# Performance work log

Hardware: AMD Instinct MI355X
Metric: run time of the kernel (lower is better)

Reference implementation:

```python
import jax, jax.numpy as jnp
import numpy as np

B, L, H, D = 1, 2048, 24, 128
HID = H * D            # 3072
MLP = 4 * HID          # 12288
EPS = 1e-6


def setup_inputs() -> dict:
    key = jax.random.key(0)
    ks = jax.random.split(key, 8)
    w = lambda k, shape: jax.random.normal(k, shape, jnp.float32) * 0.02
    return {
        "x": jax.random.normal(ks[0], (B, L, HID), jnp.float32),
        "vec": jax.random.normal(ks[1], (B, HID), jnp.float32),
        "pe": jax.random.normal(ks[2], (1, 1, L, D // 2, 2, 2), jnp.float32),
        # Modulation(double=False): Dense(3*hidden)
        "mod_w": w(ks[3], (HID, 3 * HID)),
        "mod_b": jnp.zeros((3 * HID,), jnp.float32),
        # pre_norm LayerNormalization (gamma/beta)
        "ln_gamma": jnp.ones((HID,), jnp.float32),
        "ln_beta": jnp.zeros((HID,), jnp.float32),
        # linear1: Dense(3*hidden + mlp_hidden)
        "w1": w(ks[4], (HID, 3 * HID + MLP)),
        "b1": jnp.zeros((3 * HID + MLP,), jnp.float32),
        # QKNorm scales (per head_dim)
        "q_scale": jnp.ones((D,), jnp.float32),
        "k_scale": jnp.ones((D,), jnp.float32),
        # linear2: Dense(hidden), input hidden + mlp_hidden
        "w2": w(ks[5], (HID + MLP, HID)),
        "b2": jnp.zeros((HID,), jnp.float32),
    }


def _rmsnorm(t, scale):
    # RMSNorm over last (head) dim, eps=1e-6
    return t * jax.lax.rsqrt(jnp.mean(jnp.square(t), axis=-1, keepdims=True) + EPS) * scale


def _apply_rope(t, pe):
    # t: (B,H,L,D) -> view (B,H,L,D/2,1,2); pe: (1,1,L,D/2,2,2)
    t_ = t.reshape(*t.shape[:-1], -1, 1, 2)
    out = pe[..., 0] * t_[..., 0] + pe[..., 1] * t_[..., 1]  # (B,H,L,D/2,2)
    return out.reshape(t.shape)


def reference(x, vec, pe, mod_w, mod_b, ln_gamma, ln_beta, w1, b1,
              q_scale, k_scale, w2, b2):
    # Modulation: silu -> Dense -> split into shift/scale/gate, each [B,1,HID]
    mod = (jax.nn.silu(vec) @ mod_w + mod_b)[:, None, :]
    shift, scale, gate = jnp.split(mod, 3, axis=-1)

    # pre_norm LayerNorm (eps=1e-6) + modulation affine
    mu = jnp.mean(x, axis=-1, keepdims=True)
    var = jnp.mean(jnp.square(x - mu), axis=-1, keepdims=True)
    ln = (x - mu) * jax.lax.rsqrt(var + EPS) * ln_gamma + ln_beta
    x_mod = (1.0 + scale) * ln + shift

    # linear1 -> split qkv / mlp branches
    h = x_mod @ w1 + b1
    qkv, mlp = h[..., : 3 * HID], h[..., 3 * HID:]

    # 'B L (K H D) -> K B H L D'
    qkv = qkv.reshape(B, L, 3, H, D).transpose(2, 0, 3, 1, 4)
    q, k, v = qkv[0], qkv[1], qkv[2]

    # QK RMSNorm + RoPE
    q = _apply_rope(_rmsnorm(q, q_scale), pe)
    k = _apply_rope(_rmsnorm(k, k_scale), pe)

    # scaled dot-product attention
    scores = jnp.einsum("bhqd,bhkd->bhqk", q, k) * (D ** -0.5)
    attn = jnp.einsum("bhqk,bhkd->bhqd", jax.nn.softmax(scores, axis=-1), v)
    attn = attn.transpose(0, 2, 1, 3).reshape(B, L, HID)  # B H L D -> B L (H D)

    # concat attention + gelu(mlp, tanh approx) -> linear2, gated residual
    out = jnp.concatenate([attn, jax.nn.gelu(mlp, approximate=True)], axis=-1) @ w2 + b2
    return x + gate * out
```

## Files before the change

kernel.cpp:

```cpp
#include <hip/hip_runtime.h>
#include <hip/hip_bf16.h>
#include <cstdint>

#define L_SEQ 2048
#define NH    24
#define DH    128
#define HID   3072
#define MLPD  12288
#define N1    21504
#define K2    15360
#define EPSF  1e-6f
#define ATT_SCALE 0.08838834764831845f

typedef __bf16 bf16x8 __attribute__((ext_vector_type(8)));
typedef float  f32x4  __attribute__((ext_vector_type(4)));

__device__ __forceinline__ float gelu_tanh(float x) {
    float x3 = x * x * x;
    return 0.5f * x * (1.f + tanhf(0.7978845608028654f * (x + 0.044715f * x3)));
}

__device__ __forceinline__ unsigned short f2bf(float f) {
    union { float f; unsigned int u; } x{f};
    unsigned int r = x.u + 0x7fffu + ((x.u >> 16) & 1u);
    return (unsigned short)(r >> 16);
}

__device__ __forceinline__ void gload_lds16(const void* g, void* l) {
    __builtin_amdgcn_global_load_lds(
        (__attribute__((address_space(1))) void*)g,
        (__attribute__((address_space(3))) void*)l, 16, 0, 0);
}

__global__ __launch_bounds__(256)
void k_convT(const float* __restrict__ in, unsigned short* __restrict__ out,
             int R, int C) {
    __shared__ unsigned short s[64][72];
    const int r0 = blockIdx.y * 64, c0 = blockIdx.x * 64;
    const int tid = threadIdx.x;
    const int row = tid >> 4, c4 = (tid & 15) * 4;
    #pragma unroll
    for (int rr = 0; rr < 4; rr++) {
        int r = row + rr * 16;
        float4 v = *(const float4*)&in[(size_t)(r0 + r) * C + c0 + c4];
        s[r][c4 + 0] = f2bf(v.x); s[r][c4 + 1] = f2bf(v.y);
        s[r][c4 + 2] = f2bf(v.z); s[r][c4 + 3] = f2bf(v.w);
    }
    __syncthreads();
    #pragma unroll
    for (int rr = 0; rr < 4; rr++) {
        int oc = row + rr * 16;
        ushort4 t = make_ushort4(s[c4 + 0][oc], s[c4 + 1][oc],
                                 s[c4 + 2][oc], s[c4 + 3][oc]);
        *(ushort4*)&out[(size_t)(c0 + oc) * R + r0 + c4] = t;
    }
}

__global__ __launch_bounds__(256)
void k_mod(const float* __restrict__ vec, const float* __restrict__ mod_w,
           const float* __restrict__ mod_b, float* __restrict__ mod) {
    __shared__ float sv[384];
    const int j  = blockIdx.x * 256 + threadIdx.x;
    const int k0 = blockIdx.y * 384;
    for (int i = threadIdx.x; i < 384; i += 256) {
        float v = vec[k0 + i];
        sv[i] = v / (1.f + __expf(-v));
    }
    __syncthreads();
    float acc = (blockIdx.y == 0) ? mod_b[j] : 0.f;
    #pragma unroll 8
    for (int i = 0; i < 384; i++)
        acc = fmaf(sv[i], mod_w[(size_t)(k0 + i) * 9216 + j], acc);
    atomicAdd(&mod[j], acc);
}

__global__ __launch_bounds__(256)
void k_ln(const float* __restrict__ x, const float* __restrict__ mod,
          const float* __restrict__ gamma, const float* __restrict__ beta,
          unsigned short* __restrict__ x_mod) {
    __shared__ float rs_[4], rs2_[4];
    const int l = blockIdx.x, tid = threadIdx.x;
    const float* xr = x + (size_t)l * HID;
    float s = 0.f, s2 = 0.f;
    for (int i = tid; i < HID; i += 256) {
        float v = xr[i]; s += v; s2 = fmaf(v, v, s2);
    }
    #pragma unroll
    for (int off = 32; off; off >>= 1) { s += __shfl_xor(s, off); s2 += __shfl_xor(s2, off); }
    const int w = tid >> 6;
    if ((tid & 63) == 0) { rs_[w] = s; rs2_[w] = s2; }
    __syncthreads();
    s  = rs_[0] + rs_[1] + rs_[2] + rs_[3];
    s2 = rs2_[0] + rs2_[1] + rs2_[2] + rs2_[3];
    float mu   = s * (1.f / HID);
    float var  = s2 * (1.f / HID) - mu * mu;
    float rstd = rsqrtf(var + EPSF);
    unsigned short* orow = x_mod + (size_t)l * HID;
    for (int i = tid; i < HID; i += 256) {
        float ln = (xr[i] - mu) * rstd * gamma[i] + beta[i];
        orow[i] = f2bf(fmaf(1.f + mod[HID + i], ln, mod[i]));
    }
}

template<int MODE>
__global__ __launch_bounds__(512, 2)
void gemm8(const unsigned short* __restrict__ A,
           const unsigned short* __restrict__ Bt,
           const float* __restrict__ bias, int K, int nkt,
           float* __restrict__ qkv, unsigned short* __restrict__ vt,
           unsigned short* __restrict__ a2, float* __restrict__ part) {
    extern __shared__ unsigned short sm[];
    unsigned short* As = sm;
    unsigned short* Bs = sm + 32768;
    const int tid = threadIdx.x;
    const int w = tid >> 6, lane = tid & 63;
    const int wm = w >> 2, wn = w & 3;
    const int quad = lane >> 4, lr = lane & 15;
    const int bm = blockIdx.y * 256, bn = blockIdx.x * 256;
    const int koff = (MODE == 1) ? blockIdx.z * (K >> 1) : 0;

    f32x4 acc[8][4] = {};
    bf16x8 a_[4][2], b_[2][2];

#define STG(SEL, HM, KT, D) do {                                             \
    const unsigned short* gp_ = (SEL) ? Bt : A;                              \
    const int gb_ = (SEL) ? bn : bm;                                         \
    unsigned short* ls_ = ((SEL) ? Bs : As) + (D) * 16384 + (HM) * 8192      \
                          + ((tid & ~63) << 3);                              \
    _Pragma("unroll")                                                        \
    for (int q_ = 0; q_ < 2; q_++) {                                         \
        int idx_ = q_ * 512 + tid;                                           \
        int r_   = (HM) * 128 + (idx_ >> 3);                                 \
        gload_lds16(&gp_[(size_t)(gb_ + r_) * K + koff + (KT) * 64           \
                         + (((idx_ & 7) ^ (r_ & 7)) << 3)],                  \
                    ls_ + q_ * 4096);                                        \
    }                                                                        \
} while (0)

#define LDA(MH, D) do {                                                      \
    _Pragma("unroll")                                                        \
    for (int i_ = 0; i_ < 4; i_++)                                           \
    _Pragma("unroll")                                                        \
    for (int ks_ = 0; ks_ < 2; ks_++) {                                      \
        int r_ = (MH) * 128 + i_ * 32 + wm * 16 + lr;                        \
        int c_ = ks_ * 4 + quad;                                             \
        a_[i_][ks_] = *(const bf16x8*)&As[(D) * 16384 + r_ * 64              \
                                          + ((c_ ^ (r_ & 7)) << 3)];         \
    }                                                                        \
} while (0)

#define LDB(NH, D) do {                                                      \
    _Pragma("unroll")                                                        \
    for (int j_ = 0; j_ < 2; j_++)                                           \
    _Pragma("unroll")                                                        \
    for (int ks_ = 0; ks_ < 2; ks_++) {                                      \
        int r_ = (NH) * 128 + j_ * 64 + wn * 16 + lr;                        \
        int c_ = ks_ * 4 + quad;                                             \
        b_[j_][ks_] = *(const bf16x8*)&Bs[(D) * 16384 + r_ * 64              \
                                          + ((c_ ^ (r_ & 7)) << 3)];         \
    }                                                                        \
} while (0)

#define MM(MH, NH) do {                                                      \
    __builtin_amdgcn_s_setprio(1);                                           \
    _Pragma("unroll")                                                        \
    for (int i_ = 0; i_ < 4; i_++)                                           \
    _Pragma("unroll")                                                        \
    for (int j_ = 0; j_ < 2; j_++)                                           \
    _Pragma("unroll")                                                        \
    for (int ks_ = 0; ks_ < 2; ks_++)                                        \
        acc[(MH) * 4 + i_][(NH) * 2 + j_] =                                  \
            __builtin_amdgcn_mfma_f32_16x16x32_bf16(                         \
                a_[i_][ks_], b_[j_][ks_],                                    \
                acc[(MH) * 4 + i_][(NH) * 2 + j_], 0, 0, 0);                 \
    __builtin_amdgcn_s_setprio(0);                                           \
} while (0)

#define SYNC1 do { asm volatile("s_waitcnt vmcnt(4)" ::: "memory");          \
    __builtin_amdgcn_s_barrier(); __builtin_amdgcn_sched_barrier(0); } while (0)
#define SYNC2 do { asm volatile("" ::: "memory");                            \
    __builtin_amdgcn_s_barrier(); __builtin_amdgcn_sched_barrier(0); } while (0)

    STG(0, 0, 0, 0); STG(1, 0, 0, 0); STG(0, 1, 0, 0); STG(1, 1, 0, 0);
    SYNC1;

    for (int kt = 0; kt < nkt; ++kt) {
        const int d = kt & 1, dn = d ^ 1;
        const int ktn = (kt + 1 < nkt) ? kt + 1 : 0;
        LDA(0, d); LDB(0, d);
        STG(0, 0, ktn, dn);
        SYNC1; MM(0, 0); SYNC2;
        LDA(1, d);
        STG(1, 0, ktn, dn);
        SYNC1; MM(1, 0); SYNC2;
        LDB(1, d);
        STG(0, 1, ktn, dn);
        SYNC1; MM(1, 1); SYNC2;
        LDA(0, d);
        STG(1, 1, ktn, dn);
        SYNC1; MM(0, 1); SYNC2;
    }

#undef STG
#undef LDA
#undef LDB
#undef MM
#undef SYNC1
#undef SYNC2

    float* pz = (MODE == 1) ? part + (size_t)blockIdx.z * L_SEQ * HID : nullptr;

    #pragma unroll
    for (int mh = 0; mh < 2; mh++)
    #pragma unroll
    for (int i = 0; i < 4; i++)
    #pragma unroll
    for (int nh = 0; nh < 2; nh++)
    #pragma unroll
    for (int j = 0; j < 2; j++) {
        const int col  = bn + nh * 128 + j * 64 + wn * 16 + lr;
        const int row0 = bm + mh * 128 + i * 32 + wm * 16 + quad * 4;
        const f32x4 v4 = acc[mh * 4 + i][nh * 2 + j];
        if (MODE == 0) {
            const float bs = bias[col];
            #pragma unroll
            for (int r = 0; r < 4; r++) {
                const int row = row0 + r;
                float v = v4[r] + bs;
                if (col < 2 * HID) {
                    int s3 = col / HID, rem = col - s3 * HID;
                    int hh = rem >> 7, dd = rem & 127;
                    qkv[(((size_t)s3 * NH + hh) * L_SEQ + row) * DH + dd] = v;
                } else if (col < 3 * HID) {
                    int rem = col - 2 * HID;
                    int hh = rem >> 7, dd = rem & 127;
                    vt[((size_t)hh * DH + dd) * L_SEQ + row] = f2bf(v);
                } else {
                    a2[(size_t)row * K2 + col - 6144] = f2bf(gelu_tanh(v));
                }
            }
        } else {
            #pragma unroll
            for (int r = 0; r < 4; r++)
                pz[(size_t)(row0 + r) * HID + col] = v4[r];
        }
    }
}

__global__ __launch_bounds__(256)
void k_fin(const float* __restrict__ p, const float* __restrict__ x,
           const float* __restrict__ mod, const float* __restrict__ b2,
           float* __restrict__ out) {
    const int col = blockIdx.x * 1024 + threadIdx.x * 4;
    const size_t i = (size_t)blockIdx.y * HID + col;
    float4 a  = *(const float4*)&p[i];
    float4 b  = *(const float4*)&p[(size_t)L_SEQ * HID + i];
    float4 xr = *(const float4*)&x[i];
    float4 g  = *(const float4*)&mod[2 * HID + col];
    float4 bb = *(const float4*)&b2[col];
    float4 o;
    o.x = fmaf(g.x, a.x + b.x + bb.x, xr.x);
    o.y = fmaf(g.y, a.y + b.y + bb.y, xr.y);
    o.z = fmaf(g.z, a.z + b.z + bb.z, xr.z);
    o.w = fmaf(g.w, a.w + b.w + bb.w, xr.w);
    *(float4*)&out[i] = o;
}

__global__ __launch_bounds__(64)
void k_rmsrope(const float* __restrict__ qkv, const float* __restrict__ pe,
               const float* __restrict__ qsc, const float* __restrict__ ksc,
               unsigned short* __restrict__ qb, unsigned short* __restrict__ kb) {
    const int idx = blockIdx.x;
    const int h = idx >> 11, l = idx & 2047;
    const int p = threadIdx.x;
    const float* qp = qkv + ((size_t)h * L_SEQ + l) * DH;
    const float* kp = qkv + ((size_t)(NH + h) * L_SEQ + l) * DH;
    const float4 pv = *(const float4*)&pe[((size_t)l * 64 + p) * 4];
    const float2 qs2 = *(const float2*)&qsc[2 * p];
    const float2 ks2 = *(const float2*)&ksc[2 * p];

    float2 t = *(const float2*)&qp[2 * p];
    float ss = fmaf(t.x, t.x, t.y * t.y);
    #pragma unroll
    for (int off = 32; off; off >>= 1) ss += __shfl_xor(ss, off);
    float r = rsqrtf(ss * (1.f / DH) + EPSF);
    float a = t.x * r * qs2.x, b = t.y * r * qs2.y;
    *(ushort2*)&qb[((size_t)h * L_SEQ + l) * DH + 2 * p] =
        make_ushort2(f2bf(fmaf(pv.x, a, pv.y * b) * ATT_SCALE),
                     f2bf(fmaf(pv.z, a, pv.w * b) * ATT_SCALE));

    t = *(const float2*)&kp[2 * p];
    ss = fmaf(t.x, t.x, t.y * t.y);
    #pragma unroll
    for (int off = 32; off; off >>= 1) ss += __shfl_xor(ss, off);
    r = rsqrtf(ss * (1.f / DH) + EPSF);
    a = t.x * r * ks2.x; b = t.y * r * ks2.y;
    *(ushort2*)&kb[((size_t)h * L_SEQ + l) * DH + 2 * p] =
        make_ushort2(f2bf(fmaf(pv.x, a, pv.y * b)), f2bf(fmaf(pv.z, a, pv.w * b)));
}

__global__ __launch_bounds__(256)
void attn_mfma(const unsigned short* __restrict__ qb,
               const unsigned short* __restrict__ kb,
               const unsigned short* __restrict__ vt,
               unsigned short* __restrict__ a2) {
    __shared__ unsigned short Ks[2][64 * 128];
    __shared__ unsigned short Vts[128 * 64];
    __shared__ unsigned short Ps[4][16][72];
    const int h = blockIdx.y;
    const int q0 = blockIdx.x * 64;
    const int tid = threadIdx.x;
    const int w = tid >> 6, lane = tid & 63;
    const int quad = lane >> 4, lr = lane & 15;
    const unsigned short* Qp = qb + (size_t)h * L_SEQ * DH;
    const unsigned short* Kp = kb + (size_t)h * L_SEQ * DH;
    const unsigned short* Vp = vt + (size_t)h * DH * L_SEQ;

    bf16x8 qf[4];
    #pragma unroll
    for (int c = 0; c < 4; c++)
        qf[c] = *(const bf16x8*)&Qp[(size_t)(q0 + w * 16 + lr) * DH + c * 32 + quad * 8];

    #pragma unroll
    for (int j = 0; j < 4; j++) {
        const int rb = w * 16 + j * 4;
        const int row = rb + (lane >> 4);
        const int lc = (lane & 15) ^ (row & 7);
        gload_lds16(&Kp[(size_t)row * DH + lc * 8], &Ks[0][rb * 128]);
    }

    f32x4 acc[8] = {};
    float m[4], lsum[4];
    #pragma unroll
    for (int r = 0; r < 4; r++) { m[r] = -1e30f; lsum[r] = 0.f; }

    for (int kt = 0; kt < L_SEQ; kt += 64) {
        const int d = (kt >> 6) & 1;
        const int ktn = (kt + 64 < L_SEQ) ? kt + 64 : 0;
        asm volatile("s_waitcnt vmcnt(0)" ::: "memory");
        __builtin_amdgcn_s_barrier();
        __builtin_amdgcn_sched_barrier(0);
        #pragma unroll
        for (int j = 0; j < 4; j++) {
            const int rb = w * 32 + j * 8;
            const int row = rb + (lane >> 3);
            const int lc = (lane & 7) ^ (row & 7);
            gload_lds16(&Vp[(size_t)row * L_SEQ + kt + lc * 8], &Vts[rb * 64]);
        }
        #pragma unroll
        for (int j = 0; j < 4; j++) {
            const int rb = w * 16 + j * 4;
            const int row = rb + (lane >> 4);
            const int lc = (lane & 15) ^ (row & 7);
            gload_lds16(&Kp[(size_t)(ktn + row) * DH + lc * 8], &Ks[d ^ 1][rb * 128]);
        }

        f32x4 s[4] = {};
        __builtin_amdgcn_s_setprio(1);
        #pragma unroll
        for (int c = 0; c < 4; c++) {
            #pragma unroll
            for (int n = 0; n < 4; n++) {
                const int row = n * 16 + lr;
                const bf16x8 kf = *(const bf16x8*)
                    &Ks[d][row * 128 + (((c * 4 + quad) ^ (row & 7)) * 8)];
                s[n] = __builtin_amdgcn_mfma_f32_16x16x32_bf16(qf[c], kf, s[n], 0, 0, 0);
            }
        }
        __builtin_amdgcn_s_setprio(0);

        float alpha[4];
        #pragma unroll
        for (int r = 0; r < 4; r++) {
            float t = fmaxf(fmaxf(s[0][r], s[1][r]), fmaxf(s[2][r], s[3][r]));
            t = fmaxf(t, __shfl_xor(t, 1));
            t = fmaxf(t, __shfl_xor(t, 2));
            t = fmaxf(t, __shfl_xor(t, 4));
            t = fmaxf(t, __shfl_xor(t, 8));
            const float mn = fmaxf(m[r], t);
            alpha[r] = __expf(m[r] - mn);
            m[r] = mn;
        }
        float psum[4] = {0.f, 0.f, 0.f, 0.f};
        #pragma unroll
        for (int n = 0; n < 4; n++) {
            #pragma unroll
            for (int r = 0; r < 4; r++) {
                const float p = __expf(s[n][r] - m[r]);
                psum[r] += p;
                Ps[w][quad * 4 + r][n * 16 + lr] = f2bf(p);
            }
        }
        #pragma unroll
        for (int r = 0; r < 4; r++) {
            float t = psum[r];
            t += __shfl_xor(t, 1); t += __shfl_xor(t, 2);
            t += __shfl_xor(t, 4); t += __shfl_xor(t, 8);
            lsum[r] = lsum[r] * alpha[r] + t;
        }
        #pragma unroll
        for (int dt = 0; dt < 8; dt++)
            #pragma unroll
            for (int r = 0; r < 4; r++) acc[dt][r] *= alpha[r];

        asm volatile("s_waitcnt vmcnt(4)" ::: "memory");
        __builtin_amdgcn_s_barrier();
        __builtin_amdgcn_sched_barrier(0);

        __builtin_amdgcn_s_setprio(1);
        #pragma unroll
        for (int jc = 0; jc < 2; jc++) {
            const bf16x8 pf = *(const bf16x8*)&Ps[w][lr][jc * 32 + quad * 8];
            #pragma unroll
            for (int dt = 0; dt < 8; dt++) {
                const int row = dt * 16 + lr;
                const bf16x8 vf = *(const bf16x8*)
                    &Vts[row * 64 + (((jc * 4 + quad) ^ (row & 7)) * 8)];
                acc[dt] = __builtin_amdgcn_mfma_f32_16x16x32_bf16(pf, vf, acc[dt], 0, 0, 0);
            }
        }
        __builtin_amdgcn_s_setprio(0);
    }

    float inv[4];
    #pragma unroll
    for (int r = 0; r < 4; r++) inv[r] = 1.f / lsum[r];
    unsigned short* orow = a2 + (size_t)(q0 + w * 16) * K2 + h * DH;
    #pragma unroll
    for (int dt = 0; dt < 8; dt++)
        #pragma unroll
        for (int r = 0; r < 4; r++)
            orow[(size_t)(quad * 4 + r) * K2 + dt * 16 + lr] = f2bf(acc[dt][r] * inv[r]);
}

extern "C" void kernel_launch(void* const* d_in, const int* in_sizes, int n_in,
                              void* d_out, int out_size, void* d_ws, size_t ws_size,
                              hipStream_t stream) {
    (void)in_sizes; (void)n_in; (void)out_size; (void)ws_size;
    const float* x      = (const float*)d_in[0];
    const float* vec    = (const float*)d_in[1];
    const float* pe     = (const float*)d_in[2];
    const float* mod_w  = (const float*)d_in[3];
    const float* mod_b  = (const float*)d_in[4];
    const float* gamma  = (const float*)d_in[5];
    const float* beta   = (const float*)d_in[6];
    const float* w1     = (const float*)d_in[7];
    const float* b1     = (const float*)d_in[8];
    const float* q_s    = (const float*)d_in[9];
    const float* k_s    = (const float*)d_in[10];
    const float* w2     = (const float*)d_in[11];
    const float* b2     = (const float*)d_in[12];
    float* out = (float*)d_out;

    char* ws = (char*)d_ws;
    size_t off = 0;
    float* modbuf = (float*)(ws + off);                  off += 40960;
    unsigned short* x_mod = (unsigned short*)(ws + off); off += (size_t)L_SEQ * HID * 2;
    float* qkv = (float*)(ws + off);                     off += (size_t)2 * NH * L_SEQ * DH * 4;
    unsigned short* qb  = (unsigned short*)(ws + off);   off += (size_t)NH * L_SEQ * DH * 2;
    unsigned short* kb  = (unsigned short*)(ws + off);   off += (size_t)NH * L_SEQ * DH * 2;
    unsigned short* vtb = (unsigned short*)(ws + off);   off += (size_t)NH * L_SEQ * DH * 2;
    unsigned short* a2  = (unsigned short*)(ws + off);   off += (size_t)L_SEQ * K2 * 2;
    unsigned short* w1t = (unsigned short*)(ws + off);   off += (size_t)N1 * HID * 2;
    unsigned short* w2t = (unsigned short*)(ws + off);   off += (size_t)HID * K2 * 2;
    float* part = qkv;

    static bool s_init = false;
    if (!s_init) {
        s_init = true;
        hipFuncSetAttribute(reinterpret_cast<const void*>(&gemm8<0>),
                            hipFuncAttributeMaxDynamicSharedMemorySize, 131072);
        hipFuncSetAttribute(reinterpret_cast<const void*>(&gemm8<1>),
                            hipFuncAttributeMaxDynamicSharedMemorySize, 131072);
    }

    k_convT<<<dim3(N1 / 64, HID / 64), 256, 0, stream>>>(w1, w1t, HID, N1);
    k_convT<<<dim3(HID / 64, K2 / 64), 256, 0, stream>>>(w2, w2t, K2, HID);

    hipMemsetAsync(modbuf, 0, 9216 * sizeof(float), stream);
    k_mod<<<dim3(36, 8), 256, 0, stream>>>(vec, mod_w, mod_b, modbuf);
    k_ln<<<L_SEQ, 256, 0, stream>>>(x, modbuf, gamma, beta, x_mod);

    gemm8<0><<<dim3(N1 / 256, L_SEQ / 256, 1), 512, 131072, stream>>>(
        x_mod, w1t, b1, HID, HID / 64, qkv, vtb, a2, nullptr);

    k_rmsrope<<<NH * L_SEQ, 64, 0, stream>>>(qkv, pe, q_s, k_s, qb, kb);
    attn_mfma<<<dim3(L_SEQ / 64, NH), 256, 0, stream>>>(qb, kb, vtb, a2);

    gemm8<1><<<dim3(HID / 256, L_SEQ / 256, 2), 512, 131072, stream>>>(
        a2, w2t, nullptr, K2, K2 / 2 / 64, nullptr, nullptr, nullptr, part);

    k_fin<<<dim3(HID / 1024, L_SEQ), 256, 0, stream>>>(part, x, modbuf, b2, out);
}
```

Before: 1.341 ms.

## Reorder GEMM K-loop stages to drop second barrier and remap blocks per XCD

The main GEMM kernel's inner loop is reordered so each quarter-step issues its global-to-LDS stage first, then LDS reads, then a single barrier and MFMA batch. The second barrier per quarter is removed, and B fragments are kept for both N halves in registers so the sub-tile order can change to (0,0),(0,1),(1,1),(1,0). Block indices are also remapped so consecutive blocks on each of the 8 XCDs cover contiguous tiles, which should improve L2 reuse. Dropping a barrier risks LDS write-after-read hazards, and the extra B registers raise register pressure.

Result: faster. 1.289 ms (-3.8%).

```diff
diff --git a/kernel.cpp b/kernel.cpp
--- a/kernel.cpp
+++ b/kernel.cpp
@@ -116,11 +116,19 @@
     const int w = tid >> 6, lane = tid & 63;
     const int wm = w >> 2, wn = w & 3;
     const int quad = lane >> 4, lr = lane & 15;
-    const int bm = blockIdx.y * 256, bn = blockIdx.x * 256;
-    const int koff = (MODE == 1) ? blockIdx.z * (K >> 1) : 0;
+
+    const int nbx = gridDim.x, nby = gridDim.y;
+    int f = (blockIdx.z * nby + blockIdx.y) * nbx + blockIdx.x;
+    const int cpx = (nbx * nby * gridDim.z) >> 3;
+    int sid = (f & 7) * cpx + (f >> 3);
+    const int bxi = sid % nbx; int tq = sid / nbx;
+    const int byi = tq % nby;  const int bzi = tq / nby;
+
+    const int bm = byi * 256, bn = bxi * 256;
+    const int koff = (MODE == 1) ? bzi * (K >> 1) : 0;
 
     f32x4 acc[8][4] = {};
-    bf16x8 a_[4][2], b_[2][2];
+    bf16x8 a_[4][2], b_[2][2][2];
 
 #define STG(SEL, HM, KT, D) do {                                             \
     const unsigned short* gp_ = (SEL) ? Bt : A;                              \
@@ -149,19 +157,19 @@
     }                                                                        \
 } while (0)
 
-#define LDB(NH, D) do {                                                      \
+#define LDB(NHH, D) do {                                                     \
     _Pragma("unroll")                                                        \
     for (int j_ = 0; j_ < 2; j_++)                                           \
     _Pragma("unroll")                                                        \
     for (int ks_ = 0; ks_ < 2; ks_++) {                                      \
-        int r_ = (NH) * 128 + j_ * 64 + wn * 16 + lr;                        \
+        int r_ = (NHH) * 128 + j_ * 64 + wn * 16 + lr;                       \
         int c_ = ks_ * 4 + quad;                                             \
-        b_[j_][ks_] = *(const bf16x8*)&Bs[(D) * 16384 + r_ * 64              \
-                                          + ((c_ ^ (r_ & 7)) << 3)];         \
+        b_[NHH][j_][ks_] = *(const bf16x8*)&Bs[(D) * 16384 + r_ * 64         \
+                                               + ((c_ ^ (r_ & 7)) << 3)];    \
     }                                                                        \
 } while (0)
 
-#define MM(MH, NH) do {                                                      \
+#define MM(MH, NHH) do {                                                     \
     __builtin_amdgcn_s_setprio(1);                                           \
     _Pragma("unroll")                                                        \
     for (int i_ = 0; i_ < 4; i_++)                                           \
@@ -169,46 +177,43 @@
     for (int j_ = 0; j_ < 2; j_++)                                           \
     _Pragma("unroll")                                                        \
     for (int ks_ = 0; ks_ < 2; ks_++)                                        \
-        acc[(MH) * 4 + i_][(NH) * 2 + j_] =                                  \
+        acc[(MH) * 4 + i_][(NHH) * 2 + j_] =                                 \
             __builtin_amdgcn_mfma_f32_16x16x32_bf16(                         \
-                a_[i_][ks_], b_[j_][ks_],                                    \
-                acc[(MH) * 4 + i_][(NH) * 2 + j_], 0, 0, 0);                 \
+                a_[i_][ks_], b_[NHH][j_][ks_],                               \
+                acc[(MH) * 4 + i_][(NHH) * 2 + j_], 0, 0, 0);                \
     __builtin_amdgcn_s_setprio(0);                                           \
 } while (0)
 
-#define SYNC1 do { asm volatile("s_waitcnt vmcnt(4)" ::: "memory");          \
+#define SYNC do { asm volatile("s_waitcnt vmcnt(4)" ::: "memory");           \
     __builtin_amdgcn_s_barrier(); __builtin_amdgcn_sched_barrier(0); } while (0)
-#define SYNC2 do { asm volatile("" ::: "memory");                            \
-    __builtin_amdgcn_s_barrier(); __builtin_amdgcn_sched_barrier(0); } while (0)
-
-    STG(0, 0, 0, 0); STG(1, 0, 0, 0); STG(0, 1, 0, 0); STG(1, 1, 0, 0);
-    SYNC1;
+
+    STG(0, 0, 0, 0); STG(1, 0, 0, 0); STG(1, 1, 0, 0); STG(0, 1, 0, 0);
+    SYNC;
 
     for (int kt = 0; kt < nkt; ++kt) {
         const int d = kt & 1, dn = d ^ 1;
         const int ktn = (kt + 1 < nkt) ? kt + 1 : 0;
+        STG(0, 0, ktn, dn);
         LDA(0, d); LDB(0, d);
-        STG(0, 0, ktn, dn);
-        SYNC1; MM(0, 0); SYNC2;
+        SYNC; MM(0, 0);
+        STG(1, 0, ktn, dn);
+        LDB(1, d);
+        SYNC; MM(0, 1);
+        STG(1, 1, ktn, dn);
         LDA(1, d);
-        STG(1, 0, ktn, dn);
-        SYNC1; MM(1, 0); SYNC2;
-        LDB(1, d);
+        SYNC; MM(1, 1);
         STG(0, 1, ktn, dn);
-        SYNC1; MM(1, 1); SYNC2;
-        LDA(0, d);
-        STG(1, 1, ktn, dn);
-        SYNC1; MM(0, 1); SYNC2;
-    }
+        SYNC; MM(1, 0);
+    }
+    asm volatile("s_waitcnt vmcnt(0)" ::: "memory");
 
 #undef STG
 #undef LDA
 #undef LDB
 #undef MM
-#undef SYNC1
-#undef SYNC2
-
-    float* pz = (MODE == 1) ? part + (size_t)blockIdx.z * L_SEQ * HID : nullptr;
+#undef SYNC
+
+    float* pz = (MODE == 1) ? part + (size_t)bzi * L_SEQ * HID : nullptr;
 
     #pragma unroll
     for (int mh = 0; mh < 2; mh++)
```
